# Kernel tuning notes

Measured on AMD Instinct MI355X. Metric: run time of the kernel, lower is better.

Reference implementation:

```python
import jax, jax.numpy as jnp
import numpy as np

N, E, G, H = 4096, 8192, 64, 128  # nodes, edges, graphs, hidden dim
NODE_DIM, EDGE_DIM = 11, 5


def _linear_params(key, fan_in, fan_out):
    kw, kb = jax.random.split(key)
    s = 1.0 / np.sqrt(fan_in)
    w = jax.random.uniform(kw, (fan_in, fan_out), minval=-s, maxval=s, dtype=jnp.float32)
    b = jax.random.uniform(kb, (fan_out,), minval=-s, maxval=s, dtype=jnp.float32)
    return w, b


def setup_inputs() -> dict:
    key = jax.random.key(0)
    ks = jax.random.split(key, 10)
    x = jax.random.normal(ks[0], (N, NODE_DIM), dtype=jnp.float32)
    edge_attr = jax.random.normal(ks[1], (E, EDGE_DIM), dtype=jnp.float32)
    edge_index = jax.random.randint(ks[2], (2, E), 0, N, dtype=jnp.int64)
    batch = jnp.sort(jax.random.randint(ks[3], (N,), 0, G, dtype=jnp.int64))
    # preprocess MLP: node_dim -> 128 -> 128
    p1_w, p1_b = _linear_params(ks[4], NODE_DIM, H)
    p2_w, p2_b = _linear_params(ks[5], H, H)
    # edge net: edge_dim -> 128 -> 256 -> 128 -> 128*128 (ReLU between, none after last)
    e1_w, e1_b = _linear_params(ks[6], EDGE_DIM, 128)
    e2_w, e2_b = _linear_params(ks[7], 128, 256)
    e3_w, e3_b = _linear_params(ks[8], 256, 128)
    e4_w, e4_b = _linear_params(ks[9], 128, H * H)
    return {"x": x, "edge_attr": edge_attr, "edge_index": edge_index, "batch": batch,
            "p1_w": p1_w, "p1_b": p1_b, "p2_w": p2_w, "p2_b": p2_b,
            "e1_w": e1_w, "e1_b": e1_b, "e2_w": e2_w, "e2_b": e2_b,
            "e3_w": e3_w, "e3_b": e3_b, "e4_w": e4_w, "e4_b": e4_b}


def reference(x, edge_attr, edge_index, batch,
              p1_w, p1_b, p2_w, p2_b,
              e1_w, e1_b, e2_w, e2_b, e3_w, e3_b, e4_w, e4_b):
    # node preprocess MLP (maps 11-dim features to 128 so NNConv dims are consistent)
    h = jax.nn.relu(x @ p1_w + p1_b) @ p2_w + p2_b  # [N, H]
    # edge network -> per-edge weight matrix [E, H, H]
    e = jax.nn.relu(edge_attr @ e1_w + e1_b)
    e = jax.nn.relu(e @ e2_w + e2_b)
    e = jax.nn.relu(e @ e3_w + e3_b)
    W = (e @ e4_w + e4_b).reshape(E, H, H)
    # NNConv (root_weight=False, bias=False, aggr='mean'):
    src, dst = edge_index[0], edge_index[1]
    msg = jnp.einsum('ei,eio->eo', h[src], W)  # gather + per-edge matmul, [E, H]
    agg = jax.ops.segment_sum(msg, dst, num_segments=N)
    cnt = jax.ops.segment_sum(jnp.ones((E,), msg.dtype), dst, num_segments=N)
    h_out = agg / jnp.maximum(cnt, 1.0)[:, None]  # scatter-mean, [N, H]
    # global add pool over graphs
    pooled = jax.ops.segment_sum(h_out, batch, num_segments=G)  # [G, H]
    return pooled
```

## Files before the change

### kernel.cpp

```cpp
#include <hip/hip_runtime.h>
#include <hip/hip_bf16.h>

#define N_NODES 4096
#define N_EDGES 8192
#define N_GRAPHS 64
#define HDIM 128

typedef __attribute__((ext_vector_type(8))) short bf16x8;
typedef __attribute__((ext_vector_type(4))) float f32x4;

static __device__ __forceinline__ unsigned short f2bf(float f) {
    unsigned u = __builtin_bit_cast(unsigned, f);
    u += 0x7fffu + ((u >> 16) & 1u);
    return (unsigned short)(u >> 16);
}
static __device__ __forceinline__ float bf2f(unsigned short s) {
    unsigned u = ((unsigned)s) << 16;
    return __builtin_bit_cast(float, u);
}

__global__ __launch_bounds__(256) void pre_kernel(
    const float* __restrict__ x, const float* __restrict__ p1w, const float* __restrict__ p1b,
    const float* __restrict__ p2w, const float* __restrict__ p2b, const float* __restrict__ e4b,
    unsigned short* __restrict__ h_bf, float* __restrict__ hb,
    const float* __restrict__ ea, const float* __restrict__ w1, const float* __restrict__ b1,
    const float* __restrict__ w4, unsigned short* __restrict__ w4perm,
    const float* __restrict__ w2, unsigned short* __restrict__ w2p,
    const float* __restrict__ w3, unsigned short* __restrict__ w3p,
    unsigned short* __restrict__ l1bf)
{
    __shared__ __align__(16) char smem[33024];
    const int t = threadIdx.x;
    const int bid = blockIdx.x;

    if (bid < 256) {
        float (*xs)[11]  = (float(*)[11])smem;
        float (*l1t)[16] = (float(*)[16])(smem + 704);
        float (*hs)[16]  = (float(*)[16])(smem + 8896);
        const int nb = bid;

        for (int r = t; r < 16 * 11; r += 256) {
            int e = r / 11, d = r % 11;
            xs[e][d] = x[(nb * 16 + e) * 11 + d];
        }
        __syncthreads();
        {
            int j = t & 127;
            float wd[11];
            #pragma unroll
            for (int d = 0; d < 11; ++d) wd[d] = p1w[d * 128 + j];
            float bj = p1b[j];
            for (int p = 0; p < 8; ++p) {
                int e = p * 2 + (t >> 7);
                float acc = bj;
                #pragma unroll
                for (int d = 0; d < 11; ++d) acc += xs[e][d] * wd[d];
                l1t[j][e] = fmaxf(acc, 0.f);
            }
        }
        __syncthreads();
        {
            int j = t & 127, eh = t >> 7;
            float acc[8];
            float bj = p2b[j];
            #pragma unroll
            for (int r = 0; r < 8; ++r) acc[r] = bj;
            for (int k = 0; k < 128; ++k) {
                float w = p2w[k * 128 + j];
                const float4* row = (const float4*)&l1t[k][eh * 8];
                float4 v0 = row[0], v1 = row[1];
                acc[0] += v0.x * w; acc[1] += v0.y * w; acc[2] += v0.z * w; acc[3] += v0.w * w;
                acc[4] += v1.x * w; acc[5] += v1.y * w; acc[6] += v1.z * w; acc[7] += v1.w * w;
            }
            #pragma unroll
            for (int r = 0; r < 8; ++r) {
                int e = eh * 8 + r;
                h_bf[(nb * 16 + e) * 128 + j] = f2bf(acc[r]);
                hs[j][e] = acc[r];
            }
        }
        __syncthreads();
        {
            int j = t & 127, eh = t >> 7;
            float acc[8] = {0.f,0.f,0.f,0.f,0.f,0.f,0.f,0.f};
            for (int i = 0; i < 128; ++i) {
                float w = e4b[i * 128 + j];
                const float4* row = (const float4*)&hs[i][eh * 8];
                float4 v0 = row[0], v1 = row[1];
                acc[0] += v0.x * w; acc[1] += v0.y * w; acc[2] += v0.z * w; acc[3] += v0.w * w;
                acc[4] += v1.x * w; acc[5] += v1.y * w; acc[6] += v1.z * w; acc[7] += v1.w * w;
            }
            #pragma unroll
            for (int r = 0; r < 8; ++r) hb[(nb * 16 + eh * 8 + r) * 128 + j] = acc[r];
        }
    } else if (bid < 384) {
        unsigned short (*tt)[129] = (unsigned short(*)[129])smem;
        const int i = bid - 256;
        for (int r = t; r < 16384; r += 256) {
            int k = r >> 7, o = r & 127;
            tt[o][k] = f2bf(w4[k * 16384 + i * 128 + o]);
        }
        __syncthreads();
        for (int r = t; r < 16384; r += 256) {
            int o = r >> 7, k = r & 127;
            w4perm[((size_t)(o >> 5) * 128 + i) * 4352 + (size_t)(o & 31) * 136 + k] = tt[o][k];
        }
    } else if (bid < 386) {
        unsigned short (*tt)[129] = (unsigned short(*)[129])smem;
        const int oh = bid - 384;
        for (int r = t; r < 16384; r += 256) {
            int k = r >> 7, ol = r & 127;
            tt[ol][k] = f2bf(w2[k * 256 + oh * 128 + ol]);
        }
        __syncthreads();
        for (int r = t; r < 16384; r += 256) {
            int ol = r >> 7, k = r & 127;
            w2p[(oh * 128 + ol) * 136 + k] = tt[ol][k];
        }
    } else if (bid < 388) {
        unsigned short (*tt)[257] = (unsigned short(*)[257])smem;
        const int oh = bid - 386;
        for (int r = t; r < 16384; r += 256) {
            int k = r >> 6, ol = r & 63;
            tt[ol][k] = f2bf(w3[k * 128 + oh * 64 + ol]);
        }
        __syncthreads();
        for (int r = t; r < 16384; r += 256) {
            int ol = r >> 8, k = r & 255;
            w3p[(oh * 64 + ol) * 264 + k] = tt[ol][k];
        }
    } else {
        float (*es)[5] = (float(*)[5])smem;
        const int eb = (bid - 388) * 128;
        for (int r = t; r < 640; r += 256) ((float*)es)[r] = ea[eb * 5 + r];
        __syncthreads();
        int j = t & 127, eh = t >> 7;
        float wd[5];
        #pragma unroll
        for (int d = 0; d < 5; ++d) wd[d] = w1[d * 128 + j];
        float bj = b1[j];
        for (int p = 0; p < 64; ++p) {
            int e = eh * 64 + p;
            float acc = bj;
            #pragma unroll
            for (int d = 0; d < 5; ++d) acc += es[e][d] * wd[d];
            l1bf[(size_t)(eb + e) * 128 + j] = f2bf(fmaxf(acc, 0.f));
        }
    }
}

__global__ __launch_bounds__(256, 2) void edge23_kernel(
    const unsigned short* __restrict__ l1bf,
    const float* __restrict__ b2, const float* __restrict__ b3,
    const unsigned short* __restrict__ w2p, const unsigned short* __restrict__ w3p,
    unsigned short* __restrict__ e3bf)
{
    __shared__ __align__(16) unsigned short l2a[32 * 264];
    const int t = threadIdx.x, bid = blockIdx.x;
    const int w = t >> 6, lane = t & 63, q = lane >> 4, l15 = lane & 15;
    const int e0 = bid * 32;
    const f32x4 zero4 = (f32x4){0.f, 0.f, 0.f, 0.f};

    bf16x8 afrag[2][4];
    #pragma unroll
    for (int mb = 0; mb < 2; ++mb)
        #pragma unroll
        for (int s = 0; s < 4; ++s)
            afrag[mb][s] = *(const bf16x8*)(l1bf + (size_t)(e0 + mb * 16 + l15) * 128 + s * 32 + q * 8);

    f32x4 acc[2][4];
    #pragma unroll
    for (int mb = 0; mb < 2; ++mb)
        #pragma unroll
        for (int ob = 0; ob < 4; ++ob) acc[mb][ob] = zero4;
    #pragma unroll
    for (int ob = 0; ob < 4; ++ob) {
        const int o = w * 64 + ob * 16 + l15;
        bf16x8 bfrag[4];
        #pragma unroll
        for (int s = 0; s < 4; ++s)
            bfrag[s] = *(const bf16x8*)(w2p + (size_t)o * 136 + s * 32 + q * 8);
        #pragma unroll
        for (int mb = 0; mb < 2; ++mb) {
            f32x4 tmp = __builtin_amdgcn_mfma_f32_16x16x32_bf16(afrag[mb][0], bfrag[0], zero4, 0, 0, 0);
            tmp = __builtin_amdgcn_mfma_f32_16x16x32_bf16(afrag[mb][1], bfrag[1], tmp, 0, 0, 0);
            tmp = __builtin_amdgcn_mfma_f32_16x16x32_bf16(afrag[mb][2], bfrag[2], tmp, 0, 0, 0);
            acc[mb][ob] = __builtin_amdgcn_mfma_f32_16x16x32_bf16(afrag[mb][3], bfrag[3], tmp, 0, 0, 0);
        }
    }
    #pragma unroll
    for (int mb = 0; mb < 2; ++mb)
        #pragma unroll
        for (int ob = 0; ob < 4; ++ob) {
            int o = w * 64 + ob * 16 + l15;
            float bo = b2[o];
            #pragma unroll
            for (int r = 0; r < 4; ++r) {
                int e_loc = mb * 16 + q * 4 + r;
                l2a[e_loc * 264 + o] = f2bf(fmaxf(acc[mb][ob][r] + bo, 0.f));
            }
        }
    __syncthreads();

    f32x4 acc3[2][2];
    #pragma unroll
    for (int mb = 0; mb < 2; ++mb)
        #pragma unroll
        for (int ob = 0; ob < 2; ++ob) acc3[mb][ob] = zero4;
    #pragma unroll
    for (int ks = 0; ks < 8; ++ks) {
        bf16x8 a3[2];
        #pragma unroll
        for (int mb = 0; mb < 2; ++mb)
            a3[mb] = *(const bf16x8*)&l2a[(mb * 16 + l15) * 264 + ks * 32 + q * 8];
        #pragma unroll
        for (int ob = 0; ob < 2; ++ob) {
            const int o = w * 32 + ob * 16 + l15;
            bf16x8 bf = *(const bf16x8*)(w3p + (size_t)o * 264 + ks * 32 + q * 8);
            #pragma unroll
            for (int mb = 0; mb < 2; ++mb)
                acc3[mb][ob] = __builtin_amdgcn_mfma_f32_16x16x32_bf16(a3[mb], bf, acc3[mb][ob], 0, 0, 0);
        }
    }
    #pragma unroll
    for (int mb = 0; mb < 2; ++mb)
        #pragma unroll
        for (int ob = 0; ob < 2; ++ob) {
            int o = w * 32 + ob * 16 + l15;
            float bo = b3[o];
            #pragma unroll
            for (int r = 0; r < 4; ++r) {
                int e = e0 + mb * 16 + q * 4 + r;
                e3bf[(size_t)e * 128 + o] = f2bf(fmaxf(acc3[mb][ob][r] + bo, 0.f));
            }
        }
}

__global__ __launch_bounds__(256, 3) void nnconv_kernel(
    const unsigned short* __restrict__ e3bf, const unsigned short* __restrict__ h_bf,
    const unsigned short* __restrict__ w4perm, const float* __restrict__ hb,
    const int* __restrict__ ei, float* __restrict__ agg, float* __restrict__ cnt)
{
    __shared__ __align__(16) float ht_f[64 * 64];
    __shared__ __align__(16) float red[2 * 64 * 16];
    const int t = threadIdx.x;
    const int bid = blockIdx.x;
    const int osplit = bid & 3;
    const int ksplit = (bid >> 2) & 1;
    const int etile  = bid >> 3;
    const int w = t >> 6, lane = t & 63, q = lane >> 4, l15 = lane & 15;
    const int og   = w & 1;
    const int kpar = w >> 1;
    const int e0 = etile * 64;
    const int o0 = osplit * 32;
    const int i0 = ksplit * 64;

    bf16x8 afrag[4][4];
    #pragma unroll
    for (int mb = 0; mb < 4; ++mb)
        #pragma unroll
        for (int s = 0; s < 4; ++s) {
            int row = e0 + mb * 16 + l15;
            afrag[mb][s] = *(const bf16x8*)(e3bf + (size_t)row * 128 + s * 32 + q * 8);
        }
    #pragma unroll
    for (int mb = 0; mb < 4; ++mb)
        #pragma unroll
        for (int s = 0; s < 4; ++s)
            asm volatile("" : "+v"(afrag[mb][s]));
    asm volatile("" ::: "memory");

    {
        int r = t >> 2, part = t & 3;
        int s = ei[e0 + r];
        #pragma unroll
        for (int u = 0; u < 2; ++u) {
            uint4 v = *(const uint4*)(h_bf + (size_t)s * 128 + i0 + part * 16 + u * 8);
            const unsigned short* pv = (const unsigned short*)&v;
            #pragma unroll
            for (int j = 0; j < 8; ++j)
                ht_f[(part * 16 + u * 8 + j) * 64 + r] = bf2f(pv[j]);
        }
    }

    f32x4 acc[4];
    #pragma unroll
    for (int mb = 0; mb < 4; ++mb) acc[mb] = (f32x4){0.f, 0.f, 0.f, 0.f};
    const f32x4 zero4 = (f32x4){0.f, 0.f, 0.f, 0.f};

    __syncthreads();

    const unsigned short* bbase =
        w4perm + ((size_t)osplit * 128 + i0 + kpar * 32) * 4352
               + (size_t)(og * 16 + l15) * 136 + q * 8;
    #pragma unroll 2
    for (int c = 0; c < 32; ++c) {
        const unsigned short* bp = bbase + (size_t)c * 4352;
        bf16x8 bfrag[4];
        #pragma unroll
        for (int s = 0; s < 4; ++s)
            bfrag[s] = *(const bf16x8*)(bp + s * 32);
        const int cg = kpar * 32 + c;
        #pragma unroll
        for (int mb = 0; mb < 4; ++mb) {
            f32x4 hv = *(const f32x4*)&ht_f[cg * 64 + mb * 16 + q * 4];
            f32x4 tmp = __builtin_amdgcn_mfma_f32_16x16x32_bf16(afrag[mb][0], bfrag[0], zero4, 0, 0, 0);
            tmp = __builtin_amdgcn_mfma_f32_16x16x32_bf16(afrag[mb][1], bfrag[1], tmp, 0, 0, 0);
            tmp = __builtin_amdgcn_mfma_f32_16x16x32_bf16(afrag[mb][2], bfrag[2], tmp, 0, 0, 0);
            tmp = __builtin_amdgcn_mfma_f32_16x16x32_bf16(afrag[mb][3], bfrag[3], tmp, 0, 0, 0);
            #pragma unroll
            for (int r = 0; r < 4; ++r)
                acc[mb][r] += hv[r] * tmp[r];
        }
    }

    if (kpar == 1) {
        #pragma unroll
        for (int mb = 0; mb < 4; ++mb)
            #pragma unroll
            for (int r = 0; r < 4; ++r)
                red[(og * 64 + mb * 16 + q * 4 + r) * 16 + l15] = acc[mb][r];
    }
    __syncthreads();
    if (kpar == 0) {
        #pragma unroll
        for (int mb = 0; mb < 4; ++mb) {
            #pragma unroll
            for (int r = 0; r < 4; ++r) {
                int e_loc = mb * 16 + q * 4 + r;
                int e = e0 + e_loc;
                int de = ei[N_EDGES + e];
                int se = ei[e];
                int o = o0 + og * 16 + l15;
                float v = acc[mb][r] + red[(og * 64 + e_loc) * 16 + l15];
                if (ksplit == 0) v += hb[(size_t)se * 128 + o];
                if (osplit == 0 && ksplit == 0 && og == 0 && l15 == 0)
                    atomicAdd(&cnt[de], 1.0f);
                atomicAdd(&agg[(size_t)de * 128 + o], v);
            }
        }
    }
}

__global__ __launch_bounds__(128) void pool_kernel(
    const float* __restrict__ agg, const float* __restrict__ cnt,
    const int* __restrict__ batch, float* __restrict__ out)
{
    const int g = blockIdx.x, t = threadIdx.x;
    int lo = 0, hi = N_NODES;
    while (lo < hi) { int m = (lo + hi) >> 1; if (batch[m] < g) lo = m + 1; else hi = m; }
    const int n_lo = lo;
    int lo2 = n_lo, hi2 = N_NODES;
    while (lo2 < hi2) { int m = (lo2 + hi2) >> 1; if (batch[m] < g + 1) lo2 = m + 1; else hi2 = m; }
    const int n_hi = lo2;

    float s0 = 0.f, s1 = 0.f, s2 = 0.f, s3 = 0.f;
    int n = n_lo;
    for (; n + 4 <= n_hi; n += 4) {
        float c0 = cnt[n], c1 = cnt[n + 1], c2 = cnt[n + 2], c3 = cnt[n + 3];
        float v0 = agg[(n    ) * 128 + t];
        float v1 = agg[(n + 1) * 128 + t];
        float v2 = agg[(n + 2) * 128 + t];
        float v3 = agg[(n + 3) * 128 + t];
        s0 += v0 / (c0 > 1.f ? c0 : 1.f);
        s1 += v1 / (c1 > 1.f ? c1 : 1.f);
        s2 += v2 / (c2 > 1.f ? c2 : 1.f);
        s3 += v3 / (c3 > 1.f ? c3 : 1.f);
    }
    for (; n < n_hi; ++n) {
        float c = cnt[n];
        s0 += agg[n * 128 + t] / (c > 1.f ? c : 1.f);
    }
    out[g * 128 + t] = (s0 + s1) + (s2 + s3);
}

extern "C" void kernel_launch(void* const* d_in, const int* in_sizes, int n_in,
                              void* d_out, int out_size, void* d_ws, size_t ws_size,
                              hipStream_t stream)
{
    const float* x     = (const float*)d_in[0];
    const float* ea    = (const float*)d_in[1];
    const int*   ei    = (const int*)d_in[2];
    const int*   batch = (const int*)d_in[3];
    const float* p1w   = (const float*)d_in[4];
    const float* p1b   = (const float*)d_in[5];
    const float* p2w   = (const float*)d_in[6];
    const float* p2b   = (const float*)d_in[7];
    const float* w1    = (const float*)d_in[8];
    const float* b1    = (const float*)d_in[9];
    const float* w2    = (const float*)d_in[10];
    const float* b2    = (const float*)d_in[11];
    const float* w3    = (const float*)d_in[12];
    const float* b3    = (const float*)d_in[13];
    const float* w4    = (const float*)d_in[14];
    const float* b4    = (const float*)d_in[15];
    float* out = (float*)d_out;
    (void)in_sizes; (void)n_in; (void)out_size; (void)ws_size;

    char* ws = (char*)d_ws;
    unsigned short* h_bf = (unsigned short*)(ws);
    unsigned short* e3bf = (unsigned short*)(ws + 1048576);
    float* hb            = (float*)(ws + 3145728);
    unsigned short* w4p  = (unsigned short*)(ws + 5242880);
    float* agg           = (float*)(ws + 9699328);
    unsigned short* l1bf = (unsigned short*)(ws + 9699328);
    float* cnt           = (float*)(ws + 11796480);
    unsigned short* w2p  = (unsigned short*)(ws + 11812864);
    unsigned short* w3p  = (unsigned short*)(ws + 11882496);

    pre_kernel<<<452, 256, 0, stream>>>(
        x, p1w, p1b, p2w, p2b, b4, h_bf, hb,
        ea, w1, b1, w4, w4p, w2, w2p, w3, w3p, l1bf);
    edge23_kernel<<<256, 256, 0, stream>>>(l1bf, b2, b3, w2p, w3p, e3bf);
    hipMemsetAsync(agg, 0, (size_t)N_NODES * 128 * 4 + (size_t)N_NODES * 4, stream);
    nnconv_kernel<<<1024, 256, 0, stream>>>(e3bf, h_bf, w4p, hb, ei, agg, cnt);
    pool_kernel<<<N_GRAPHS, 128, 0, stream>>>(agg, cnt, batch, out);
}
```

Before: 179.3 us.

## Retile NNConv to 128-edge tiles with full-K per block and B prefetch

The nnconv kernel now gives each block 128 edges and 16 output columns, and drops the K split so the four waves each own a quarter of the 128 input features. Partial sums are reduced through shared memory, and the gathered node features are kept as bf16 in LDS. The w4 fragments for the next chunk are software-prefetched while the current one runs. This doubles reuse of each loaded w4perm fragment across edges and halves the grid, at the cost of more registers (occupancy hint lowered from 3 to 2), a larger LDS footprint and fewer blocks.

```diff
diff --git a/kernel.cpp b/kernel.cpp
--- a/kernel.cpp
+++ b/kernel.cpp
@@ -8,6 +8,7 @@
 
 typedef __attribute__((ext_vector_type(8))) short bf16x8;
 typedef __attribute__((ext_vector_type(4))) float f32x4;
+typedef __attribute__((ext_vector_type(4))) unsigned short u16x4;
 
 static __device__ __forceinline__ unsigned short f2bf(float f) {
     unsigned u = __builtin_bit_cast(unsigned, f);
@@ -236,106 +237,109 @@
         }
 }
 
-__global__ __launch_bounds__(256, 3) void nnconv_kernel(
+__global__ __launch_bounds__(256, 2) void nnconv_kernel(
     const unsigned short* __restrict__ e3bf, const unsigned short* __restrict__ h_bf,
     const unsigned short* __restrict__ w4perm, const float* __restrict__ hb,
     const int* __restrict__ ei, float* __restrict__ agg, float* __restrict__ cnt)
 {
-    __shared__ __align__(16) float ht_f[64 * 64];
-    __shared__ __align__(16) float red[2 * 64 * 16];
+    __shared__ __align__(16) unsigned short ht[128 * 128];
+    __shared__ __align__(16) float red[3 * 128 * 16];
     const int t = threadIdx.x;
     const int bid = blockIdx.x;
-    const int osplit = bid & 3;
-    const int ksplit = (bid >> 2) & 1;
+    const int osplit = bid & 7;
     const int etile  = bid >> 3;
     const int w = t >> 6, lane = t & 63, q = lane >> 4, l15 = lane & 15;
-    const int og   = w & 1;
-    const int kpar = w >> 1;
-    const int e0 = etile * 64;
-    const int o0 = osplit * 32;
-    const int i0 = ksplit * 64;
-
-    bf16x8 afrag[4][4];
-    #pragma unroll
-    for (int mb = 0; mb < 4; ++mb)
+    const int kpar = w;
+    const int e0 = etile * 128;
+    const int o0 = osplit * 16;
+
+    bf16x8 afrag[8][4];
+    #pragma unroll
+    for (int mb = 0; mb < 8; ++mb)
         #pragma unroll
         for (int s = 0; s < 4; ++s) {
             int row = e0 + mb * 16 + l15;
             afrag[mb][s] = *(const bf16x8*)(e3bf + (size_t)row * 128 + s * 32 + q * 8);
         }
     #pragma unroll
-    for (int mb = 0; mb < 4; ++mb)
+    for (int mb = 0; mb < 8; ++mb)
         #pragma unroll
         for (int s = 0; s < 4; ++s)
             asm volatile("" : "+v"(afrag[mb][s]));
     asm volatile("" ::: "memory");
 
     {
-        int r = t >> 2, part = t & 3;
+        int r = t >> 1, part = t & 1;
         int s = ei[e0 + r];
         #pragma unroll
-        for (int u = 0; u < 2; ++u) {
-            uint4 v = *(const uint4*)(h_bf + (size_t)s * 128 + i0 + part * 16 + u * 8);
+        for (int u = 0; u < 8; ++u) {
+            uint4 v = *(const uint4*)(h_bf + (size_t)s * 128 + part * 64 + u * 8);
             const unsigned short* pv = (const unsigned short*)&v;
             #pragma unroll
             for (int j = 0; j < 8; ++j)
-                ht_f[(part * 16 + u * 8 + j) * 64 + r] = bf2f(pv[j]);
-        }
-    }
-
-    f32x4 acc[4];
-    #pragma unroll
-    for (int mb = 0; mb < 4; ++mb) acc[mb] = (f32x4){0.f, 0.f, 0.f, 0.f};
+                ht[(part * 64 + u * 8 + j) * 128 + r] = pv[j];
+        }
+    }
+
+    f32x4 acc[8];
+    #pragma unroll
+    for (int mb = 0; mb < 8; ++mb) acc[mb] = (f32x4){0.f, 0.f, 0.f, 0.f};
     const f32x4 zero4 = (f32x4){0.f, 0.f, 0.f, 0.f};
 
     __syncthreads();
 
     const unsigned short* bbase =
-        w4perm + ((size_t)osplit * 128 + i0 + kpar * 32) * 4352
-               + (size_t)(og * 16 + l15) * 136 + q * 8;
-    #pragma unroll 2
+        w4perm + ((size_t)(osplit >> 1) * 128 + kpar * 32) * 4352
+               + (size_t)((osplit & 1) * 16 + l15) * 136 + q * 8;
+    bf16x8 bcur[4], bnxt[4];
+    #pragma unroll
+    for (int s = 0; s < 4; ++s) bcur[s] = *(const bf16x8*)(bbase + s * 32);
     for (int c = 0; c < 32; ++c) {
-        const unsigned short* bp = bbase + (size_t)c * 4352;
-        bf16x8 bfrag[4];
-        #pragma unroll
-        for (int s = 0; s < 4; ++s)
-            bfrag[s] = *(const bf16x8*)(bp + s * 32);
-        const int cg = kpar * 32 + c;
-        #pragma unroll
-        for (int mb = 0; mb < 4; ++mb) {
-            f32x4 hv = *(const f32x4*)&ht_f[cg * 64 + mb * 16 + q * 4];
-            f32x4 tmp = __builtin_amdgcn_mfma_f32_16x16x32_bf16(afrag[mb][0], bfrag[0], zero4, 0, 0, 0);
-            tmp = __builtin_amdgcn_mfma_f32_16x16x32_bf16(afrag[mb][1], bfrag[1], tmp, 0, 0, 0);
-            tmp = __builtin_amdgcn_mfma_f32_16x16x32_bf16(afrag[mb][2], bfrag[2], tmp, 0, 0, 0);
-            tmp = __builtin_amdgcn_mfma_f32_16x16x32_bf16(afrag[mb][3], bfrag[3], tmp, 0, 0, 0);
+        if (c + 1 < 32) {
+            const unsigned short* bp = bbase + (size_t)(c + 1) * 4352;
+            #pragma unroll
+            for (int s = 0; s < 4; ++s) bnxt[s] = *(const bf16x8*)(bp + s * 32);
+        }
+        const int gi = kpar * 32 + c;
+        #pragma unroll
+        for (int mb = 0; mb < 8; ++mb) {
+            u16x4 hr = *(const u16x4*)&ht[gi * 128 + mb * 16 + q * 4];
+            f32x4 tmp = __builtin_amdgcn_mfma_f32_16x16x32_bf16(afrag[mb][0], bcur[0], zero4, 0, 0, 0);
+            tmp = __builtin_amdgcn_mfma_f32_16x16x32_bf16(afrag[mb][1], bcur[1], tmp, 0, 0, 0);
+            tmp = __builtin_amdgcn_mfma_f32_16x16x32_bf16(afrag[mb][2], bcur[2], tmp, 0, 0, 0);
+            tmp = __builtin_amdgcn_mfma_f32_16x16x32_bf16(afrag[mb][3], bcur[3], tmp, 0, 0, 0);
             #pragma unroll
             for (int r = 0; r < 4; ++r)
-                acc[mb][r] += hv[r] * tmp[r];
-        }
-    }
-
-    if (kpar == 1) {
-        #pragma unroll
-        for (int mb = 0; mb < 4; ++mb)
+                acc[mb][r] += bf2f(hr[r]) * tmp[r];
+        }
+        #pragma unroll
+        for (int s = 0; s < 4; ++s) bcur[s] = bnxt[s];
+    }
+
+    if (w > 0) {
+        #pragma unroll
+        for (int mb = 0; mb < 8; ++mb)
             #pragma unroll
             for (int r = 0; r < 4; ++r)
-                red[(og * 64 + mb * 16 + q * 4 + r) * 16 + l15] = acc[mb][r];
+                red[((w - 1) * 128 + mb * 16 + q * 4 + r) * 16 + l15] = acc[mb][r];
     }
     __syncthreads();
-    if (kpar == 0) {
-        #pragma unroll
-        for (int mb = 0; mb < 4; ++mb) {
+    if (w == 0) {
+        #pragma unroll
+        for (int mb = 0; mb < 8; ++mb) {
             #pragma unroll
             for (int r = 0; r < 4; ++r) {
                 int e_loc = mb * 16 + q * 4 + r;
                 int e = e0 + e_loc;
                 int de = ei[N_EDGES + e];
                 int se = ei[e];
-                int o = o0 + og * 16 + l15;
-                float v = acc[mb][r] + red[(og * 64 + e_loc) * 16 + l15];
-                if (ksplit == 0) v += hb[(size_t)se * 128 + o];
-                if (osplit == 0 && ksplit == 0 && og == 0 && l15 == 0)
-                    atomicAdd(&cnt[de], 1.0f);
+                int o = o0 + l15;
+                float v = acc[mb][r]
+                        + red[(0 * 128 + e_loc) * 16 + l15]
+                        + red[(1 * 128 + e_loc) * 16 + l15]
+                        + red[(2 * 128 + e_loc) * 16 + l15]
+                        + hb[(size_t)se * 128 + o];
+                if (osplit == 0 && l15 == 0) atomicAdd(&cnt[de], 1.0f);
                 atomicAdd(&agg[(size_t)de * 128 + o], v);
             }
         }
@@ -413,6 +417,6 @@
         ea, w1, b1, w4, w4p, w2, w2p, w3, w3p, l1bf);
     edge23_kernel<<<256, 256, 0, stream>>>(l1bf, b2, b3, w2p, w3p, e3bf);
     hipMemsetAsync(agg, 0, (size_t)N_NODES * 128 * 4 + (size_t)N_NODES * 4, stream);
-    nnconv_kernel<<<1024, 256, 0, stream>>>(e3bf, h_bf, w4p, hb, ei, agg, cnt);
+    nnconv_kernel<<<512, 256, 0, stream>>>(e3bf, h_bf, w4p, hb, ei, agg, cnt);
     pool_kernel<<<N_GRAPHS, 128, 0, stream>>>(agg, cnt, batch, out);
 }
```

Measured after the change: 182.9 us. +2.0%, slower.

## Fuse edge layer-1 into edge23 kernel, shrink edge tile, fold agg zeroing

Applied to the files above, without the earlier changes.

Edge-net layer 1 moves out of pre_kernel into edge23_kernel. Its bf16 output now stays in shared memory instead of a global l1bf buffer. The edge tile per block drops from 32 to 16 edges, so 512 blocks run instead of 256, and 128 extra blocks zero agg/cnt in place of the separate hipMemsetAsync. The p2/e4b inner loops also get unroll pragmas. This removes a global round trip and a launch, but each block now reloads the w2/w3 fragments for half as many edges, doubling weight traffic.

```diff
diff --git a/kernel.cpp b/kernel.cpp
--- a/kernel.cpp
+++ b/kernel.cpp
@@ -23,11 +23,9 @@
     const float* __restrict__ x, const float* __restrict__ p1w, const float* __restrict__ p1b,
     const float* __restrict__ p2w, const float* __restrict__ p2b, const float* __restrict__ e4b,
     unsigned short* __restrict__ h_bf, float* __restrict__ hb,
-    const float* __restrict__ ea, const float* __restrict__ w1, const float* __restrict__ b1,
     const float* __restrict__ w4, unsigned short* __restrict__ w4perm,
     const float* __restrict__ w2, unsigned short* __restrict__ w2p,
-    const float* __restrict__ w3, unsigned short* __restrict__ w3p,
-    unsigned short* __restrict__ l1bf)
+    const float* __restrict__ w3, unsigned short* __restrict__ w3p)
 {
     __shared__ __align__(16) char smem[33024];
     const int t = threadIdx.x;
@@ -65,6 +63,7 @@
             float bj = p2b[j];
             #pragma unroll
             for (int r = 0; r < 8; ++r) acc[r] = bj;
+            #pragma unroll 8
             for (int k = 0; k < 128; ++k) {
                 float w = p2w[k * 128 + j];
                 const float4* row = (const float4*)&l1t[k][eh * 8];
@@ -83,6 +82,7 @@
         {
             int j = t & 127, eh = t >> 7;
             float acc[8] = {0.f,0.f,0.f,0.f,0.f,0.f,0.f,0.f};
+            #pragma unroll 8
             for (int i = 0; i < 128; ++i) {
                 float w = e4b[i * 128 + j];
                 const float4* row = (const float4*)&hs[i][eh * 8];
@@ -117,7 +117,7 @@
             int ol = r >> 7, k = r & 127;
             w2p[(oh * 128 + ol) * 136 + k] = tt[ol][k];
         }
-    } else if (bid < 388) {
+    } else {
         unsigned short (*tt)[257] = (unsigned short(*)[257])smem;
         const int oh = bid - 386;
         for (int r = t; r < 16384; r += 256) {
@@ -129,50 +129,58 @@
             int ol = r >> 8, k = r & 255;
             w3p[(oh * 64 + ol) * 264 + k] = tt[ol][k];
         }
-    } else {
-        float (*es)[5] = (float(*)[5])smem;
-        const int eb = (bid - 388) * 128;
-        for (int r = t; r < 640; r += 256) ((float*)es)[r] = ea[eb * 5 + r];
-        __syncthreads();
+    }
+}
+
+__global__ __launch_bounds__(256, 2) void edge23_kernel(
+    const float* __restrict__ ea, const float* __restrict__ w1, const float* __restrict__ b1,
+    const float* __restrict__ b2, const float* __restrict__ b3,
+    const unsigned short* __restrict__ w2p, const unsigned short* __restrict__ w3p,
+    unsigned short* __restrict__ e3bf, float* __restrict__ aggz)
+{
+    const int t = threadIdx.x, bid = blockIdx.x;
+
+    if (bid >= 512) {
+        float4* dst = (float4*)aggz;
+        const float4 z = make_float4(0.f, 0.f, 0.f, 0.f);
+        for (int i = (bid - 512) * 256 + t; i < 132096; i += 128 * 256) dst[i] = z;
+        return;
+    }
+
+    __shared__ __align__(16) float es[16][5];
+    __shared__ __align__(16) unsigned short l1a[16 * 136];
+    __shared__ __align__(16) unsigned short l2a[16 * 264];
+    const int w = t >> 6, lane = t & 63, q = lane >> 4, l15 = lane & 15;
+    const int e0 = bid * 16;
+    const f32x4 zero4 = (f32x4){0.f, 0.f, 0.f, 0.f};
+
+    for (int r = t; r < 80; r += 256) es[r / 5][r % 5] = ea[e0 * 5 + r];
+    __syncthreads();
+    {
         int j = t & 127, eh = t >> 7;
         float wd[5];
         #pragma unroll
         for (int d = 0; d < 5; ++d) wd[d] = w1[d * 128 + j];
         float bj = b1[j];
-        for (int p = 0; p < 64; ++p) {
-            int e = eh * 64 + p;
+        #pragma unroll
+        for (int p = 0; p < 8; ++p) {
+            int e = eh * 8 + p;
             float acc = bj;
             #pragma unroll
             for (int d = 0; d < 5; ++d) acc += es[e][d] * wd[d];
-            l1bf[(size_t)(eb + e) * 128 + j] = f2bf(fmaxf(acc, 0.f));
-        }
-    }
-}
-
-__global__ __launch_bounds__(256, 2) void edge23_kernel(
-    const unsigned short* __restrict__ l1bf,
-    const float* __restrict__ b2, const float* __restrict__ b3,
-    const unsigned short* __restrict__ w2p, const unsigned short* __restrict__ w3p,
-    unsigned short* __restrict__ e3bf)
-{
-    __shared__ __align__(16) unsigned short l2a[32 * 264];
-    const int t = threadIdx.x, bid = blockIdx.x;
-    const int w = t >> 6, lane = t & 63, q = lane >> 4, l15 = lane & 15;
-    const int e0 = bid * 32;
-    const f32x4 zero4 = (f32x4){0.f, 0.f, 0.f, 0.f};
-
-    bf16x8 afrag[2][4];
-    #pragma unroll
-    for (int mb = 0; mb < 2; ++mb)
-        #pragma unroll
-        for (int s = 0; s < 4; ++s)
-            afrag[mb][s] = *(const bf16x8*)(l1bf + (size_t)(e0 + mb * 16 + l15) * 128 + s * 32 + q * 8);
-
-    f32x4 acc[2][4];
-    #pragma unroll
-    for (int mb = 0; mb < 2; ++mb)
-        #pragma unroll
-        for (int ob = 0; ob < 4; ++ob) acc[mb][ob] = zero4;
+            l1a[e * 136 + j] = f2bf(fmaxf(acc, 0.f));
+        }
+    }
+    __syncthreads();
+
+    bf16x8 afrag[4];
+    #pragma unroll
+    for (int s = 0; s < 4; ++s)
+        afrag[s] = *(const bf16x8*)&l1a[l15 * 136 + s * 32 + q * 8];
+
+    f32x4 acc[4];
+    #pragma unroll
+    for (int ob = 0; ob < 4; ++ob) acc[ob] = zero4;
     #pragma unroll
     for (int ob = 0; ob < 4; ++ob) {
         const int o = w * 64 + ob * 16 + l15;
@@ -180,60 +188,45 @@
         #pragma unroll
         for (int s = 0; s < 4; ++s)
             bfrag[s] = *(const bf16x8*)(w2p + (size_t)o * 136 + s * 32 + q * 8);
-        #pragma unroll
-        for (int mb = 0; mb < 2; ++mb) {
-            f32x4 tmp = __builtin_amdgcn_mfma_f32_16x16x32_bf16(afrag[mb][0], bfrag[0], zero4, 0, 0, 0);
-            tmp = __builtin_amdgcn_mfma_f32_16x16x32_bf16(afrag[mb][1], bfrag[1], tmp, 0, 0, 0);
-            tmp = __builtin_amdgcn_mfma_f32_16x16x32_bf16(afrag[mb][2], bfrag[2], tmp, 0, 0, 0);
-            acc[mb][ob] = __builtin_amdgcn_mfma_f32_16x16x32_bf16(afrag[mb][3], bfrag[3], tmp, 0, 0, 0);
-        }
-    }
-    #pragma unroll
-    for (int mb = 0; mb < 2; ++mb)
-        #pragma unroll
-        for (int ob = 0; ob < 4; ++ob) {
-            int o = w * 64 + ob * 16 + l15;
-            float bo = b2[o];
-            #pragma unroll
-            for (int r = 0; r < 4; ++r) {
-                int e_loc = mb * 16 + q * 4 + r;
-                l2a[e_loc * 264 + o] = f2bf(fmaxf(acc[mb][ob][r] + bo, 0.f));
-            }
-        }
+        f32x4 tmp = __builtin_amdgcn_mfma_f32_16x16x32_bf16(afrag[0], bfrag[0], zero4, 0, 0, 0);
+        tmp = __builtin_amdgcn_mfma_f32_16x16x32_bf16(afrag[1], bfrag[1], tmp, 0, 0, 0);
+        tmp = __builtin_amdgcn_mfma_f32_16x16x32_bf16(afrag[2], bfrag[2], tmp, 0, 0, 0);
+        acc[ob] = __builtin_amdgcn_mfma_f32_16x16x32_bf16(afrag[3], bfrag[3], tmp, 0, 0, 0);
+    }
+    #pragma unroll
+    for (int ob = 0; ob < 4; ++ob) {
+        int o = w * 64 + ob * 16 + l15;
+        float bo = b2[o];
+        #pragma unroll
+        for (int r = 0; r < 4; ++r) {
+            int e_loc = q * 4 + r;
+            l2a[e_loc * 264 + o] = f2bf(fmaxf(acc[ob][r] + bo, 0.f));
+        }
+    }
     __syncthreads();
 
-    f32x4 acc3[2][2];
-    #pragma unroll
-    for (int mb = 0; mb < 2; ++mb)
-        #pragma unroll
-        for (int ob = 0; ob < 2; ++ob) acc3[mb][ob] = zero4;
+    f32x4 acc3[2];
+    acc3[0] = zero4; acc3[1] = zero4;
     #pragma unroll
     for (int ks = 0; ks < 8; ++ks) {
-        bf16x8 a3[2];
-        #pragma unroll
-        for (int mb = 0; mb < 2; ++mb)
-            a3[mb] = *(const bf16x8*)&l2a[(mb * 16 + l15) * 264 + ks * 32 + q * 8];
+        bf16x8 a3 = *(const bf16x8*)&l2a[l15 * 264 + ks * 32 + q * 8];
         #pragma unroll
         for (int ob = 0; ob < 2; ++ob) {
             const int o = w * 32 + ob * 16 + l15;
             bf16x8 bf = *(const bf16x8*)(w3p + (size_t)o * 264 + ks * 32 + q * 8);
-            #pragma unroll
-            for (int mb = 0; mb < 2; ++mb)
-                acc3[mb][ob] = __builtin_amdgcn_mfma_f32_16x16x32_bf16(a3[mb], bf, acc3[mb][ob], 0, 0, 0);
-        }
-    }
-    #pragma unroll
-    for (int mb = 0; mb < 2; ++mb)
-        #pragma unroll
-        for (int ob = 0; ob < 2; ++ob) {
-            int o = w * 32 + ob * 16 + l15;
-            float bo = b3[o];
-            #pragma unroll
-            for (int r = 0; r < 4; ++r) {
-                int e = e0 + mb * 16 + q * 4 + r;
-                e3bf[(size_t)e * 128 + o] = f2bf(fmaxf(acc3[mb][ob][r] + bo, 0.f));
-            }
-        }
+            acc3[ob] = __builtin_amdgcn_mfma_f32_16x16x32_bf16(a3, bf, acc3[ob], 0, 0, 0);
+        }
+    }
+    #pragma unroll
+    for (int ob = 0; ob < 2; ++ob) {
+        int o = w * 32 + ob * 16 + l15;
+        float bo = b3[o];
+        #pragma unroll
+        for (int r = 0; r < 4; ++r) {
+            int e = e0 + q * 4 + r;
+            e3bf[(size_t)e * 128 + o] = f2bf(fmaxf(acc3[ob][r] + bo, 0.f));
+        }
+    }
 }
 
 __global__ __launch_bounds__(256, 3) void nnconv_kernel(
@@ -403,16 +396,14 @@
     float* hb            = (float*)(ws + 3145728);
     unsigned short* w4p  = (unsigned short*)(ws + 5242880);
     float* agg           = (float*)(ws + 9699328);
-    unsigned short* l1bf = (unsigned short*)(ws + 9699328);
     float* cnt           = (float*)(ws + 11796480);
     unsigned short* w2p  = (unsigned short*)(ws + 11812864);
     unsigned short* w3p  = (unsigned short*)(ws + 11882496);
 
-    pre_kernel<<<452, 256, 0, stream>>>(
+    pre_kernel<<<388, 256, 0, stream>>>(
         x, p1w, p1b, p2w, p2b, b4, h_bf, hb,
-        ea, w1, b1, w4, w4p, w2, w2p, w3, w3p, l1bf);
-    edge23_kernel<<<256, 256, 0, stream>>>(l1bf, b2, b3, w2p, w3p, e3bf);
-    hipMemsetAsync(agg, 0, (size_t)N_NODES * 128 * 4 + (size_t)N_NODES * 4, stream);
+        w4, w4p, w2, w2p, w3, w3p);
+    edge23_kernel<<<640, 256, 0, stream>>>(ea, w1, b1, b2, b3, w2p, w3p, e3bf, agg);
     nnconv_kernel<<<1024, 256, 0, stream>>>(e3bf, h_bf, w4p, hb, ei, agg, cnt);
     pool_kernel<<<N_GRAPHS, 128, 0, stream>>>(agg, cnt, batch, out);
 }
```

New measurement: 176.3 us. About the same (-1.7%).
